# Kernel tuning notes

Measured on AMD Instinct MI355X. Metric: run time of the kernel, lower is better.

## Reference

```python
import jax, jax.numpy as jnp
import numpy as np

B, N, C, H, TR = 2, 5000, 256, 8, 2
M = N // TR  # reduced KV length from Conv1d(data_len, data_len//tr, 1)
DK = C // H


def setup_inputs() -> dict:
    key = jax.random.key(0)
    ks = jax.random.split(key, 10)
    s = 0.02
    return {
        "x": jax.random.normal(ks[0], (B, N, C), jnp.float32),
        "Wq": jax.random.normal(ks[1], (C, C), jnp.float32) * s,
        "bq": jnp.zeros((C,), jnp.float32),
        "Wk": jax.random.normal(ks[2], (C, C), jnp.float32) * s,
        "bk": jnp.zeros((C,), jnp.float32),
        "Wv": jax.random.normal(ks[3], (C, C), jnp.float32) * s,
        "bv": jnp.zeros((C,), jnp.float32),
        "Wc": jax.random.normal(ks[4], (M, N), jnp.float32) * (1.0 / np.sqrt(N)),
        "bc": jnp.zeros((M,), jnp.float32),
        "gamma": jnp.ones((C,), jnp.float32),
        "beta": jnp.zeros((C,), jnp.float32),
    }


def _layernorm(x, gamma, beta, eps=1e-5):
    mu = jnp.mean(x, axis=-1, keepdims=True)
    var = jnp.mean(jnp.square(x - mu), axis=-1, keepdims=True)
    return gamma * (x - mu) * jax.lax.rsqrt(var + eps) + beta


def reference(x, Wq, bq, Wk, bk, Wv, bv, Wc, bc, gamma, beta):
    b, n, c = x.shape
    # Q projection: (B, H, N, DK)
    q = (x @ Wq.T + bq).reshape(b, n, H, DK).transpose(0, 2, 1, 3)
    # Spatial reduction: Conv1d with kernel size 1 over the N (channel) dim,
    # then LayerNorm over feature dim C
    x_ = jnp.einsum('mn,bnc->bmc', Wc, x) + bc[None, :, None]
    x_ = _layernorm(x_, gamma, beta)
    k = (x_ @ Wk.T + bk).reshape(b, -1, H, DK).transpose(0, 2, 1, 3)  # (B,H,M,DK)
    v = (x_ @ Wv.T + bv).reshape(b, -1, H, DK).transpose(0, 2, 1, 3)  # (B,H,M,DK)
    # Naive attention (full score matrix, as in the original module)
    scores = jnp.einsum('bhnd,bhmd->bhnm', q, k) / jnp.sqrt(jnp.asarray(DK, x.dtype))
    p = jax.nn.softmax(scores, axis=-1)
    out = jnp.einsum('bhnm,bhmd->bhnd', p, v)
    # note: output_linear is declared in __init__ but never applied in forward
    return out.transpose(0, 2, 1, 3).reshape(b, n, c)
```

## Files before the change

kernel.cpp:

```cpp
#include <hip/hip_runtime.h>
#include <hip/hip_bf16.h>
#include <hip/hip_fp16.h>
#include <math.h>

constexpr int B = 2;
constexpr int N = 5000;
constexpr int C = 256;
constexpr int H = 8;
constexpr int DK = 32;
constexpr int M = 2500;
constexpr int MP = 2512;
constexpr int KSTEPS = 157;
constexpr int SPLIT = 8;
constexpr int MTILES = 79;
constexpr float QSCALE = 0.2550598692503365f;

typedef __attribute__((ext_vector_type(8))) short bf16x8;
typedef __attribute__((ext_vector_type(4))) float f32x4;

static __device__ __forceinline__ ushort f2bf(float f) {
  __hip_bfloat16 h = __float2bfloat16(f);
  return *reinterpret_cast<ushort*>(&h);
}

static __device__ __forceinline__ float fastexp2(float x) {
#if __has_builtin(__builtin_amdgcn_exp2f)
  return __builtin_amdgcn_exp2f(x);
#else
  return exp2f(x);
#endif
}

__global__ __launch_bounds__(256) void wcast(const float* __restrict__ Wq,
                                             const float* __restrict__ Wk,
                                             const float* __restrict__ Wv,
                                             ushort* __restrict__ W16) {
  const float* src = (blockIdx.y == 0) ? Wq : (blockIdx.y == 1) ? Wk : Wv;
  const int idx = blockIdx.x * 1024 + threadIdx.x * 4;
  const float4 v = *reinterpret_cast<const float4*>(src + idx);
  ushort4 o;
  o.x = f2bf(v.x); o.y = f2bf(v.y); o.z = f2bf(v.z); o.w = f2bf(v.w);
  *reinterpret_cast<ushort4*>(W16 + (size_t)blockIdx.y * C * C + idx) = o;
}

__global__ __launch_bounds__(256) void xt_cast(const float* __restrict__ x,
                                               ushort* __restrict__ xTt,
                                               ushort* __restrict__ xb16) {
  const int n0 = blockIdx.x * 64, c0 = blockIdx.y * 64, b = blockIdx.z;
  const int tid = threadIdx.x;
  __shared__ ushort T[64][68];
  const float* xb = x + (size_t)b * N * C;
#pragma unroll
  for (int i = 0; i < 4; ++i) {
    const int nl = (tid >> 4) + i * 16;
    const int cg = (tid & 15) * 4;
    float4 v = {0.f, 0.f, 0.f, 0.f};
    const bool ok = (n0 + nl) < N;
    if (ok) v = *reinterpret_cast<const float4*>(xb + (size_t)(n0 + nl) * C + c0 + cg);
    ushort4 u;
    u.x = f2bf(v.x); u.y = f2bf(v.y); u.z = f2bf(v.z); u.w = f2bf(v.w);
    T[nl][cg + 0] = u.x; T[nl][cg + 1] = u.y; T[nl][cg + 2] = u.z; T[nl][cg + 3] = u.w;
    if (ok)
      *reinterpret_cast<ushort4*>(xb16 + ((size_t)b * N + n0 + nl) * C + c0 + cg) = u;
  }
  __syncthreads();
  ushort* ob = xTt + (size_t)b * KSTEPS * C * 32;
  const int cl = tid & 63, ng = tid >> 6;
#pragma unroll
  for (int j = 0; j < 2; ++j) {
    const int nstart = ng * 16 + j * 8;
    const int n = n0 + nstart;
    if (n >= KSTEPS * 32) continue;
    const int ks = n >> 5, kk = n & 31;
    ushort vals[8];
#pragma unroll
    for (int jj = 0; jj < 8; ++jj) vals[jj] = T[nstart + jj][cl];
    *reinterpret_cast<bf16x8*>(ob + ((size_t)ks * C + (c0 + cl)) * 32 + kk) =
        *reinterpret_cast<const bf16x8*>(vals);
  }
}

__global__ __launch_bounds__(256) void conv_mfma(const float* __restrict__ Wc,
                                                 const ushort* __restrict__ xTt,
                                                 ushort* __restrict__ xpart) {
  const int s = blockIdx.x & 7;
  const int mt = blockIdx.x >> 3;
  const int m0 = mt * 32;
  const int tid = threadIdx.x, w = tid >> 6, l = tid & 63;
  const int lr = l & 15, lg = l >> 4;
  f32x4 acc[16];
#pragma unroll
  for (int i = 0; i < 16; ++i) acc[i] = (f32x4){0.f, 0.f, 0.f, 0.f};
  const int row0 = m0 + lr, row1 = m0 + 16 + lr;
  const bool ok0 = row0 < M, ok1 = row1 < M;
  const float* ap0 = Wc + (size_t)(ok0 ? row0 : 0) * N + lg * 8;
  const float* ap1 = Wc + (size_t)(ok1 ? row1 : 0) * N + lg * 8;
  const int crow = w * 64 + lr;

#pragma unroll 2
  for (int ks = s; ks < KSTEPS; ks += SPLIT) {
    const int n0 = ks * 32;
    const bool kok = (n0 + lg * 8) < N;
    bf16x8 a0 = {0, 0, 0, 0, 0, 0, 0, 0}, a1 = {0, 0, 0, 0, 0, 0, 0, 0};
    if (ok0 && kok) {
      const float4 v0 = *reinterpret_cast<const float4*>(ap0 + n0);
      const float4 v1 = *reinterpret_cast<const float4*>(ap0 + n0 + 4);
      ushort u[8];
      u[0] = f2bf(v0.x); u[1] = f2bf(v0.y); u[2] = f2bf(v0.z); u[3] = f2bf(v0.w);
      u[4] = f2bf(v1.x); u[5] = f2bf(v1.y); u[6] = f2bf(v1.z); u[7] = f2bf(v1.w);
      a0 = *reinterpret_cast<const bf16x8*>(u);
    }
    if (ok1 && kok) {
      const float4 v0 = *reinterpret_cast<const float4*>(ap1 + n0);
      const float4 v1 = *reinterpret_cast<const float4*>(ap1 + n0 + 4);
      ushort u[8];
      u[0] = f2bf(v0.x); u[1] = f2bf(v0.y); u[2] = f2bf(v0.z); u[3] = f2bf(v0.w);
      u[4] = f2bf(v1.x); u[5] = f2bf(v1.y); u[6] = f2bf(v1.z); u[7] = f2bf(v1.w);
      a1 = *reinterpret_cast<const bf16x8*>(u);
    }
    bf16x8 bf[8];
#pragma unroll
    for (int ct = 0; ct < 4; ++ct)
#pragma unroll
      for (int bb = 0; bb < 2; ++bb)
        bf[ct * 2 + bb] = *reinterpret_cast<const bf16x8*>(
            xTt + (((size_t)bb * KSTEPS + ks) * C + crow + ct * 16) * 32 + lg * 8);
#pragma unroll
    for (int ct = 0; ct < 4; ++ct)
#pragma unroll
      for (int bb = 0; bb < 2; ++bb) {
        acc[(0 * 4 + ct) * 2 + bb] =
            __builtin_amdgcn_mfma_f32_16x16x32_bf16(a0, bf[ct * 2 + bb], acc[(0 * 4 + ct) * 2 + bb], 0, 0, 0);
        acc[(1 * 4 + ct) * 2 + bb] =
            __builtin_amdgcn_mfma_f32_16x16x32_bf16(a1, bf[ct * 2 + bb], acc[(1 * 4 + ct) * 2 + bb], 0, 0, 0);
      }
  }

#pragma unroll
  for (int mf = 0; mf < 2; ++mf)
#pragma unroll
    for (int ct = 0; ct < 4; ++ct)
#pragma unroll
      for (int bb = 0; bb < 2; ++bb)
#pragma unroll
        for (int i = 0; i < 4; ++i) {
          const int m = m0 + mf * 16 + lg * 4 + i;
          if (m < M) {
            const __half hv = __float2half(acc[(mf * 4 + ct) * 2 + bb][i]);
            xpart[(((size_t)s * B + bb) * M + m) * C + w * 64 + ct * 16 + lr] =
                *reinterpret_cast<const ushort*>(&hv);
          }
        }
}

__global__ __launch_bounds__(256) void ln_kernel(const ushort* __restrict__ xp,
                                                 const float* __restrict__ bc,
                                                 const float* __restrict__ gamma,
                                                 const float* __restrict__ beta,
                                                 ushort* __restrict__ xr16) {
  const int row = blockIdx.x;
  const int tid = threadIdx.x;
  const int b = row / M, m = row - b * M;
  const size_t base = (size_t)row * C;
  float v = bc[m];
#pragma unroll
  for (int s = 0; s < SPLIT; ++s) {
    const ushort us = xp[(((size_t)s * B + b) * M + m) * C + tid];
    v += __half2float(*reinterpret_cast<const __half*>(&us));
  }
  __shared__ float red[8];
  float sum = v;
#pragma unroll
  for (int o = 32; o >= 1; o >>= 1) sum += __shfl_xor(sum, o);
  if ((tid & 63) == 0) red[tid >> 6] = sum;
  __syncthreads();
  const float mu = (red[0] + red[1] + red[2] + red[3]) * (1.f / C);
  const float d = v - mu;
  float s2 = d * d;
#pragma unroll
  for (int o = 32; o >= 1; o >>= 1) s2 += __shfl_xor(s2, o);
  if ((tid & 63) == 0) red[4 + (tid >> 6)] = s2;
  __syncthreads();
  const float var = (red[4] + red[5] + red[6] + red[7]) * (1.f / C);
  xr16[base + tid] = f2bf(gamma[tid] * d * rsqrtf(var + 1e-5f) + beta[tid]);
}

__global__ __launch_bounds__(256) void proj_all(const ushort* __restrict__ xb16,
                                                const ushort* __restrict__ xr16,
                                                const ushort* __restrict__ W16,
                                                const float* __restrict__ bq,
                                                const float* __restrict__ bk,
                                                const float* __restrict__ bv,
                                                ushort* __restrict__ qb,
                                                ushort* __restrict__ kb,
                                                ushort* __restrict__ vt) {
  const int z = blockIdx.z;
  const int R = (z == 0) ? N : M;
  const int totalRows = B * R;
  if (blockIdx.x * 64 >= totalRows) return;
  const ushort* xin = (z == 0) ? xb16 : xr16;
  const ushort* W = W16 + (size_t)z * C * C;
  const float* bias = (z == 0) ? bq : (z == 1) ? bk : bv;
  const int tid = threadIdx.x, w = tid >> 6, l = tid & 63;
  const int lr = l & 15, lg = l >> 4;
  const int r0 = blockIdx.x * 64 + w * 16;
  const int c0 = blockIdx.y * 64;
  const int arow = r0 + lr;
  const bool aok = arow < totalRows;
  f32x4 acc[4] = {{0.f,0.f,0.f,0.f},{0.f,0.f,0.f,0.f},{0.f,0.f,0.f,0.f},{0.f,0.f,0.f,0.f}};
#pragma unroll
  for (int ks = 0; ks < 8; ++ks) {
    bf16x8 af = {0, 0, 0, 0, 0, 0, 0, 0};
    if (aok) af = *reinterpret_cast<const bf16x8*>(xin + (size_t)arow * C + ks * 32 + lg * 8);
#pragma unroll
    for (int ct = 0; ct < 4; ++ct) {
      const bf16x8 bf =
          *reinterpret_cast<const bf16x8*>(W + (size_t)(c0 + ct * 16 + lr) * C + ks * 32 + lg * 8);
      acc[ct] = __builtin_amdgcn_mfma_f32_16x16x32_bf16(af, bf, acc[ct], 0, 0, 0);
    }
  }
#pragma unroll
  for (int ct = 0; ct < 4; ++ct) {
    const int c = c0 + ct * 16 + lr;
    const int h = c >> 5, d = c & 31;
    const float bi = bias[c];
#pragma unroll
    for (int i = 0; i < 4; ++i) {
      const int row = r0 + lg * 4 + i;
      if (row >= totalRows) continue;
      const int bb = (row >= R) ? 1 : 0;
      const int rr = row - bb * R;
      float val = acc[ct][i] + bi;
      if (z == 0) {
        val *= QSCALE;
        qb[(((size_t)bb * H + h) * N + rr) * DK + d] = f2bf(val);
      } else if (z == 1) {
        kb[(((size_t)bb * H + h) * M + rr) * DK + d] = f2bf(val);
      } else {
        vt[(((size_t)bb * H + h) * DK + d) * MP + rr] = f2bf(val);
      }
    }
  }
}

__global__ __launch_bounds__(256) void attn9(const ushort* __restrict__ q,
                                             const ushort* __restrict__ kk,
                                             const ushort* __restrict__ vt,
                                             float* __restrict__ o0,
                                             float* __restrict__ o1,
                                             float* __restrict__ ps0,
                                             float* __restrict__ ps1) {
  const int qt = blockIdx.x, h = blockIdx.y, z = blockIdx.z;
  const int b = z >> 1, half = z & 1;
  const int tid = threadIdx.x, w = tid >> 6, l = tid & 63;
  const int lr = l & 15, lg = l >> 4;
  const int n0 = qt * 128 + w * 32;
  __shared__ ushort Plds[4][2][16][72];
  const ushort* qp = q + (size_t)(b * H + h) * N * DK;
  const ushort* kp = kk + (size_t)(b * H + h) * M * DK;
  const ushort* vp = vt + (size_t)(b * H + h) * DK * MP;
  float* op = half ? o1 : o0;
  float* ps = half ? ps1 : ps0;

  bf16x8 qf0 = {0, 0, 0, 0, 0, 0, 0, 0}, qf1 = {0, 0, 0, 0, 0, 0, 0, 0};
  if (n0 + lr < N) qf0 = *reinterpret_cast<const bf16x8*>(qp + (size_t)(n0 + lr) * DK + lg * 8);
  if (n0 + 16 + lr < N)
    qf1 = *reinterpret_cast<const bf16x8*>(qp + (size_t)(n0 + 16 + lr) * DK + lg * 8);

  f32x4 O0[2] = {{0.f, 0.f, 0.f, 0.f}, {0.f, 0.f, 0.f, 0.f}};
  f32x4 O1[2] = {{0.f, 0.f, 0.f, 0.f}, {0.f, 0.f, 0.f, 0.f}};
  float ps0r = 0.f, ps1r = 0.f;

  const int tbeg = half ? 20 : 0;
  const int tend = half ? 40 : 20;
#pragma unroll 1
  for (int t = tbeg; t < tend; ++t) {
    const int m0 = t * 64;
    const bool full = (m0 + 64) <= M;
    bf16x8 kf[4];
#pragma unroll
    for (int ct = 0; ct < 4; ++ct) {
      const int mr = m0 + ct * 16 + lr;
      if (full || mr < M)
        kf[ct] = *reinterpret_cast<const bf16x8*>(kp + (size_t)mr * DK + lg * 8);
      else
        kf[ct] = (bf16x8){0, 0, 0, 0, 0, 0, 0, 0};
    }
    bf16x8 vf[4];
#pragma unroll
    for (int dt = 0; dt < 2; ++dt) {
      const ushort* vb = vp + (size_t)(dt * 16 + lr) * MP + m0 + lg * 8;
      vf[dt * 2 + 0] = *reinterpret_cast<const bf16x8*>(vb);
      vf[dt * 2 + 1] = *reinterpret_cast<const bf16x8*>(vb + 32);
    }
#pragma unroll
    for (int ct = 0; ct < 4; ++ct) {
      const f32x4 s0 =
          __builtin_amdgcn_mfma_f32_16x16x32_bf16(kf[ct], qf0, (f32x4){0.f, 0.f, 0.f, 0.f}, 0, 0, 0);
      const f32x4 s1 =
          __builtin_amdgcn_mfma_f32_16x16x32_bf16(kf[ct], qf1, (f32x4){0.f, 0.f, 0.f, 0.f}, 0, 0, 0);
      float p0[4], p1[4];
#pragma unroll
      for (int i = 0; i < 4; ++i) {
        const bool mok = full || (m0 + ct * 16 + lg * 4 + i) < M;
        p0[i] = mok ? fastexp2(s0[i]) : 0.f;
        p1[i] = mok ? fastexp2(s1[i]) : 0.f;
        ps0r += p0[i];
        ps1r += p1[i];
      }
      __hip_bfloat162 a01 = __float22bfloat162_rn(make_float2(p0[0], p0[1]));
      __hip_bfloat162 a23 = __float22bfloat162_rn(make_float2(p0[2], p0[3]));
      uint2 u0;
      u0.x = *reinterpret_cast<unsigned*>(&a01);
      u0.y = *reinterpret_cast<unsigned*>(&a23);
      *reinterpret_cast<uint2*>(&Plds[w][0][lr][ct * 16 + lg * 4]) = u0;
      __hip_bfloat162 b01 = __float22bfloat162_rn(make_float2(p1[0], p1[1]));
      __hip_bfloat162 b23 = __float22bfloat162_rn(make_float2(p1[2], p1[3]));
      uint2 u1;
      u1.x = *reinterpret_cast<unsigned*>(&b01);
      u1.y = *reinterpret_cast<unsigned*>(&b23);
      *reinterpret_cast<uint2*>(&Plds[w][1][lr][ct * 16 + lg * 4]) = u1;
    }
    const bf16x8 pa00 = *reinterpret_cast<const bf16x8*>(&Plds[w][0][lr][lg * 8]);
    const bf16x8 pa01 = *reinterpret_cast<const bf16x8*>(&Plds[w][0][lr][32 + lg * 8]);
    const bf16x8 pa10 = *reinterpret_cast<const bf16x8*>(&Plds[w][1][lr][lg * 8]);
    const bf16x8 pa11 = *reinterpret_cast<const bf16x8*>(&Plds[w][1][lr][32 + lg * 8]);
#pragma unroll
    for (int dt = 0; dt < 2; ++dt) {
      O0[dt] = __builtin_amdgcn_mfma_f32_16x16x32_bf16(pa00, vf[dt * 2 + 0], O0[dt], 0, 0, 0);
      O0[dt] = __builtin_amdgcn_mfma_f32_16x16x32_bf16(pa01, vf[dt * 2 + 1], O0[dt], 0, 0, 0);
      O1[dt] = __builtin_amdgcn_mfma_f32_16x16x32_bf16(pa10, vf[dt * 2 + 0], O1[dt], 0, 0, 0);
      O1[dt] = __builtin_amdgcn_mfma_f32_16x16x32_bf16(pa11, vf[dt * 2 + 1], O1[dt], 0, 0, 0);
    }
  }

  ps0r += __shfl_xor(ps0r, 16);
  ps0r += __shfl_xor(ps0r, 32);
  ps1r += __shfl_xor(ps1r, 16);
  ps1r += __shfl_xor(ps1r, 32);
  if (lg == 0) {
    const size_t pbase = ((size_t)b * H + h) * N;
    if (n0 + lr < N) ps[pbase + n0 + lr] = ps0r;
    if (n0 + 16 + lr < N) ps[pbase + n0 + 16 + lr] = ps1r;
  }
#pragma unroll
  for (int i = 0; i < 4; ++i) {
    const int r0q = n0 + lg * 4 + i;
    const int r1q = n0 + 16 + lg * 4 + i;
    if (r0q < N) {
      float* ob = op + ((size_t)b * N + r0q) * C + h * DK + lr;
      ob[0] = O0[0][i];
      ob[16] = O0[1][i];
    }
    if (r1q < N) {
      float* ob = op + ((size_t)b * N + r1q) * C + h * DK + lr;
      ob[0] = O1[0][i];
      ob[16] = O1[1][i];
    }
  }
}

__global__ __launch_bounds__(256) void attn_combine(float* __restrict__ out,
                                                    const float* __restrict__ o1,
                                                    const float* __restrict__ ps0,
                                                    const float* __restrict__ ps1) {
  const int row = blockIdx.x;
  const int c = threadIdx.x;
  const int b = row / N, n = row - b * N;
  const size_t pidx = ((size_t)b * H + (c >> 5)) * N + n;
  const float denom = ps0[pidx] + ps1[pidx];
  const size_t idx = (size_t)row * C + c;
  out[idx] = (out[idx] + o1[idx]) / denom;
}

extern "C" void kernel_launch(void* const* d_in, const int* in_sizes, int n_in,
                              void* d_out, int out_size, void* d_ws, size_t ws_size,
                              hipStream_t stream) {
  (void)in_sizes; (void)n_in; (void)out_size; (void)ws_size;
  const float* x     = (const float*)d_in[0];
  const float* Wq    = (const float*)d_in[1];
  const float* bq    = (const float*)d_in[2];
  const float* Wk    = (const float*)d_in[3];
  const float* bk    = (const float*)d_in[4];
  const float* Wv    = (const float*)d_in[5];
  const float* bv    = (const float*)d_in[6];
  const float* Wc    = (const float*)d_in[7];
  const float* bc    = (const float*)d_in[8];
  const float* gamma = (const float*)d_in[9];
  const float* beta  = (const float*)d_in[10];
  float* out = (float*)d_out;

  char* wsb = (char*)d_ws;
  ushort* xpart = (ushort*)wsb;
  ushort* qb = (ushort*)wsb;
  ushort* kb = (ushort*)(wsb + 5120000);
  ushort* vt = (ushort*)(wsb + 7680000);
  float* ps0 = (float*)(wsb + 10400000);
  float* ps1 = (float*)(wsb + 10720000);
  char* p = wsb + 20480000;
  ushort* xTt  = (ushort*)p;
  ushort* xr16 = (ushort*)p;
  float* o1 = (float*)p;
  p += 5144576;
  ushort* xb16 = (ushort*)p; p += 5120000;
  ushort* W16  = (ushort*)p;

  wcast<<<dim3(64, 3), 256, 0, stream>>>(Wq, Wk, Wv, W16);
  xt_cast<<<dim3((N + 63) / 64, C / 64, B), 256, 0, stream>>>(x, xTt, xb16);
  conv_mfma<<<dim3(MTILES * SPLIT), 256, 0, stream>>>(Wc, xTt, xpart);
  ln_kernel<<<dim3(B * M), 256, 0, stream>>>(xpart, bc, gamma, beta, xr16);
  (void)hipMemsetAsync(vt, 0, (size_t)B * H * DK * MP * 2 + 4096, stream);
  proj_all<<<dim3((B * N + 63) / 64, C / 64, 3), 256, 0, stream>>>(xb16, xr16, W16, bq, bk, bv,
                                                                   qb, kb, vt);
  attn9<<<dim3((N + 127) / 128, H, B * 2), 256, 0, stream>>>(qb, kb, vt, out, o1, ps0, ps1);
  attn_combine<<<dim3(B * N), 256, 0, stream>>>(out, o1, ps0, ps1);
}
```

Measured before the change: 177.6 us.

## Compute softmax row sums via MFMA with ones row; peel tail tile; widen conv blocks

The attention kernel appends a row of ones to the transposed V buffer, so the P·V MFMA also produces the softmax denominators. This replaces the per-element scalar sums and cross-lane shuffles. The main loop now handles only full 64-wide KV tiles without bounds masks, and the partial last tile is peeled out into a separate block. The conv kernel uses 512-thread blocks, each wave covering 32 channels instead of 64, which halves its accumulator registers. The cost is extra MFMAs, a larger V buffer, one extra small kernel to write the ones row, and a bigger memset.

```diff
diff --git a/kernel.cpp b/kernel.cpp
--- a/kernel.cpp
+++ b/kernel.cpp
@@ -10,6 +10,7 @@
 constexpr int DK = 32;
 constexpr int M = 2500;
 constexpr int MP = 2512;
+constexpr int VROWS = 48;
 constexpr int KSTEPS = 157;
 constexpr int SPLIT = 8;
 constexpr int MTILES = 79;
@@ -41,6 +42,12 @@
   ushort4 o;
   o.x = f2bf(v.x); o.y = f2bf(v.y); o.z = f2bf(v.z); o.w = f2bf(v.w);
   *reinterpret_cast<ushort4*>(W16 + (size_t)blockIdx.y * C * C + idx) = o;
+}
+
+__global__ __launch_bounds__(256) void vt_ones(ushort* __restrict__ vt) {
+  const int bh = blockIdx.y;
+  const int j = blockIdx.x * 256 + threadIdx.x;
+  if (j < MP) vt[((size_t)bh * VROWS + 32) * MP + j] = 0x3F80;
 }
 
 __global__ __launch_bounds__(256) void xt_cast(const float* __restrict__ x,
@@ -80,7 +87,7 @@
   }
 }
 
-__global__ __launch_bounds__(256) void conv_mfma(const float* __restrict__ Wc,
+__global__ __launch_bounds__(512) void conv_mfma(const float* __restrict__ Wc,
                                                  const ushort* __restrict__ xTt,
                                                  ushort* __restrict__ xpart) {
   const int s = blockIdx.x & 7;
@@ -88,14 +95,14 @@
   const int m0 = mt * 32;
   const int tid = threadIdx.x, w = tid >> 6, l = tid & 63;
   const int lr = l & 15, lg = l >> 4;
-  f32x4 acc[16];
-#pragma unroll
-  for (int i = 0; i < 16; ++i) acc[i] = (f32x4){0.f, 0.f, 0.f, 0.f};
+  f32x4 acc[8];
+#pragma unroll
+  for (int i = 0; i < 8; ++i) acc[i] = (f32x4){0.f, 0.f, 0.f, 0.f};
   const int row0 = m0 + lr, row1 = m0 + 16 + lr;
   const bool ok0 = row0 < M, ok1 = row1 < M;
   const float* ap0 = Wc + (size_t)(ok0 ? row0 : 0) * N + lg * 8;
   const float* ap1 = Wc + (size_t)(ok1 ? row1 : 0) * N + lg * 8;
-  const int crow = w * 64 + lr;
+  const int crow = w * 32 + lr;
 
 #pragma unroll 2
   for (int ks = s; ks < KSTEPS; ks += SPLIT) {
@@ -118,36 +125,36 @@
       u[4] = f2bf(v1.x); u[5] = f2bf(v1.y); u[6] = f2bf(v1.z); u[7] = f2bf(v1.w);
       a1 = *reinterpret_cast<const bf16x8*>(u);
     }
-    bf16x8 bf[8];
-#pragma unroll
-    for (int ct = 0; ct < 4; ++ct)
+    bf16x8 bf[4];
+#pragma unroll
+    for (int ct = 0; ct < 2; ++ct)
 #pragma unroll
       for (int bb = 0; bb < 2; ++bb)
         bf[ct * 2 + bb] = *reinterpret_cast<const bf16x8*>(
             xTt + (((size_t)bb * KSTEPS + ks) * C + crow + ct * 16) * 32 + lg * 8);
 #pragma unroll
-    for (int ct = 0; ct < 4; ++ct)
+    for (int ct = 0; ct < 2; ++ct)
 #pragma unroll
       for (int bb = 0; bb < 2; ++bb) {
-        acc[(0 * 4 + ct) * 2 + bb] =
-            __builtin_amdgcn_mfma_f32_16x16x32_bf16(a0, bf[ct * 2 + bb], acc[(0 * 4 + ct) * 2 + bb], 0, 0, 0);
-        acc[(1 * 4 + ct) * 2 + bb] =
-            __builtin_amdgcn_mfma_f32_16x16x32_bf16(a1, bf[ct * 2 + bb], acc[(1 * 4 + ct) * 2 + bb], 0, 0, 0);
+        acc[(0 * 2 + ct) * 2 + bb] =
+            __builtin_amdgcn_mfma_f32_16x16x32_bf16(a0, bf[ct * 2 + bb], acc[(0 * 2 + ct) * 2 + bb], 0, 0, 0);
+        acc[(1 * 2 + ct) * 2 + bb] =
+            __builtin_amdgcn_mfma_f32_16x16x32_bf16(a1, bf[ct * 2 + bb], acc[(1 * 2 + ct) * 2 + bb], 0, 0, 0);
       }
   }
 
 #pragma unroll
   for (int mf = 0; mf < 2; ++mf)
 #pragma unroll
-    for (int ct = 0; ct < 4; ++ct)
+    for (int ct = 0; ct < 2; ++ct)
 #pragma unroll
       for (int bb = 0; bb < 2; ++bb)
 #pragma unroll
         for (int i = 0; i < 4; ++i) {
           const int m = m0 + mf * 16 + lg * 4 + i;
           if (m < M) {
-            const __half hv = __float2half(acc[(mf * 4 + ct) * 2 + bb][i]);
-            xpart[(((size_t)s * B + bb) * M + m) * C + w * 64 + ct * 16 + lr] =
+            const __half hv = __float2half(acc[(mf * 2 + ct) * 2 + bb][i]);
+            xpart[(((size_t)s * B + bb) * M + m) * C + w * 32 + ct * 16 + lr] =
                 *reinterpret_cast<const ushort*>(&hv);
           }
         }
@@ -237,19 +244,19 @@
       } else if (z == 1) {
         kb[(((size_t)bb * H + h) * M + rr) * DK + d] = f2bf(val);
       } else {
-        vt[(((size_t)bb * H + h) * DK + d) * MP + rr] = f2bf(val);
+        vt[(((size_t)bb * H + h) * VROWS + d) * MP + rr] = f2bf(val);
       }
     }
   }
 }
 
-__global__ __launch_bounds__(256) void attn9(const ushort* __restrict__ q,
-                                             const ushort* __restrict__ kk,
-                                             const ushort* __restrict__ vt,
-                                             float* __restrict__ o0,
-                                             float* __restrict__ o1,
-                                             float* __restrict__ ps0,
-                                             float* __restrict__ ps1) {
+__global__ __launch_bounds__(256) void attn10(const ushort* __restrict__ q,
+                                              const ushort* __restrict__ kk,
+                                              const ushort* __restrict__ vt,
+                                              float* __restrict__ o0,
+                                              float* __restrict__ o1,
+                                              float* __restrict__ ps0,
+                                              float* __restrict__ ps1) {
   const int qt = blockIdx.x, h = blockIdx.y, z = blockIdx.z;
   const int b = z >> 1, half = z & 1;
   const int tid = threadIdx.x, w = tid >> 6, l = tid & 63;
@@ -258,7 +265,7 @@
   __shared__ ushort Plds[4][2][16][72];
   const ushort* qp = q + (size_t)(b * H + h) * N * DK;
   const ushort* kp = kk + (size_t)(b * H + h) * M * DK;
-  const ushort* vp = vt + (size_t)(b * H + h) * DK * MP;
+  const ushort* vp = vt + (size_t)(b * H + h) * VROWS * MP;
   float* op = half ? o1 : o0;
   float* ps = half ? ps1 : ps0;
 
@@ -269,29 +276,85 @@
 
   f32x4 O0[2] = {{0.f, 0.f, 0.f, 0.f}, {0.f, 0.f, 0.f, 0.f}};
   f32x4 O1[2] = {{0.f, 0.f, 0.f, 0.f}, {0.f, 0.f, 0.f, 0.f}};
-  float ps0r = 0.f, ps1r = 0.f;
+  f32x4 O2a = {0.f, 0.f, 0.f, 0.f}, O2b = {0.f, 0.f, 0.f, 0.f};
 
   const int tbeg = half ? 20 : 0;
-  const int tend = half ? 40 : 20;
+  const int tendf = half ? 39 : 20;
 #pragma unroll 1
-  for (int t = tbeg; t < tend; ++t) {
+  for (int t = tbeg; t < tendf; ++t) {
     const int m0 = t * 64;
-    const bool full = (m0 + 64) <= M;
     bf16x8 kf[4];
 #pragma unroll
-    for (int ct = 0; ct < 4; ++ct) {
-      const int mr = m0 + ct * 16 + lr;
-      if (full || mr < M)
-        kf[ct] = *reinterpret_cast<const bf16x8*>(kp + (size_t)mr * DK + lg * 8);
-      else
-        kf[ct] = (bf16x8){0, 0, 0, 0, 0, 0, 0, 0};
-    }
-    bf16x8 vf[4];
+    for (int ct = 0; ct < 4; ++ct)
+      kf[ct] = *reinterpret_cast<const bf16x8*>(kp + (size_t)(m0 + ct * 16 + lr) * DK + lg * 8);
+    bf16x8 vf[4], vf2[2];
 #pragma unroll
     for (int dt = 0; dt < 2; ++dt) {
       const ushort* vb = vp + (size_t)(dt * 16 + lr) * MP + m0 + lg * 8;
       vf[dt * 2 + 0] = *reinterpret_cast<const bf16x8*>(vb);
       vf[dt * 2 + 1] = *reinterpret_cast<const bf16x8*>(vb + 32);
+    }
+    {
+      const ushort* vb2 = vp + (size_t)(32 + lr) * MP + m0 + lg * 8;
+      vf2[0] = *reinterpret_cast<const bf16x8*>(vb2);
+      vf2[1] = *reinterpret_cast<const bf16x8*>(vb2 + 32);
+    }
+#pragma unroll
+    for (int ct = 0; ct < 4; ++ct) {
+      const f32x4 s0 =
+          __builtin_amdgcn_mfma_f32_16x16x32_bf16(kf[ct], qf0, (f32x4){0.f, 0.f, 0.f, 0.f}, 0, 0, 0);
+      const f32x4 s1 =
+          __builtin_amdgcn_mfma_f32_16x16x32_bf16(kf[ct], qf1, (f32x4){0.f, 0.f, 0.f, 0.f}, 0, 0, 0);
+      __hip_bfloat162 a01 = __float22bfloat162_rn(make_float2(fastexp2(s0[0]), fastexp2(s0[1])));
+      __hip_bfloat162 a23 = __float22bfloat162_rn(make_float2(fastexp2(s0[2]), fastexp2(s0[3])));
+      uint2 u0;
+      u0.x = *reinterpret_cast<unsigned*>(&a01);
+      u0.y = *reinterpret_cast<unsigned*>(&a23);
+      *reinterpret_cast<uint2*>(&Plds[w][0][lr][ct * 16 + lg * 4]) = u0;
+      __hip_bfloat162 b01 = __float22bfloat162_rn(make_float2(fastexp2(s1[0]), fastexp2(s1[1])));
+      __hip_bfloat162 b23 = __float22bfloat162_rn(make_float2(fastexp2(s1[2]), fastexp2(s1[3])));
+      uint2 u1;
+      u1.x = *reinterpret_cast<unsigned*>(&b01);
+      u1.y = *reinterpret_cast<unsigned*>(&b23);
+      *reinterpret_cast<uint2*>(&Plds[w][1][lr][ct * 16 + lg * 4]) = u1;
+    }
+    const bf16x8 pa00 = *reinterpret_cast<const bf16x8*>(&Plds[w][0][lr][lg * 8]);
+    const bf16x8 pa01 = *reinterpret_cast<const bf16x8*>(&Plds[w][0][lr][32 + lg * 8]);
+    const bf16x8 pa10 = *reinterpret_cast<const bf16x8*>(&Plds[w][1][lr][lg * 8]);
+    const bf16x8 pa11 = *reinterpret_cast<const bf16x8*>(&Plds[w][1][lr][32 + lg * 8]);
+#pragma unroll
+    for (int dt = 0; dt < 2; ++dt) {
+      O0[dt] = __builtin_amdgcn_mfma_f32_16x16x32_bf16(pa00, vf[dt * 2 + 0], O0[dt], 0, 0, 0);
+      O0[dt] = __builtin_amdgcn_mfma_f32_16x16x32_bf16(pa01, vf[dt * 2 + 1], O0[dt], 0, 0, 0);
+      O1[dt] = __builtin_amdgcn_mfma_f32_16x16x32_bf16(pa10, vf[dt * 2 + 0], O1[dt], 0, 0, 0);
+      O1[dt] = __builtin_amdgcn_mfma_f32_16x16x32_bf16(pa11, vf[dt * 2 + 1], O1[dt], 0, 0, 0);
+    }
+    O2a = __builtin_amdgcn_mfma_f32_16x16x32_bf16(pa00, vf2[0], O2a, 0, 0, 0);
+    O2a = __builtin_amdgcn_mfma_f32_16x16x32_bf16(pa01, vf2[1], O2a, 0, 0, 0);
+    O2b = __builtin_amdgcn_mfma_f32_16x16x32_bf16(pa10, vf2[0], O2b, 0, 0, 0);
+    O2b = __builtin_amdgcn_mfma_f32_16x16x32_bf16(pa11, vf2[1], O2b, 0, 0, 0);
+  }
+
+  if (half) {
+    const int m0 = 39 * 64;
+    bf16x8 kf[4];
+#pragma unroll
+    for (int ct = 0; ct < 4; ++ct) {
+      const int mr = m0 + ct * 16 + lr;
+      kf[ct] = (bf16x8){0, 0, 0, 0, 0, 0, 0, 0};
+      if (mr < M) kf[ct] = *reinterpret_cast<const bf16x8*>(kp + (size_t)mr * DK + lg * 8);
+    }
+    bf16x8 vf[4], vf2[2];
+#pragma unroll
+    for (int dt = 0; dt < 2; ++dt) {
+      const ushort* vb = vp + (size_t)(dt * 16 + lr) * MP + m0 + lg * 8;
+      vf[dt * 2 + 0] = *reinterpret_cast<const bf16x8*>(vb);
+      vf[dt * 2 + 1] = *reinterpret_cast<const bf16x8*>(vb + 32);
+    }
+    {
+      const ushort* vb2 = vp + (size_t)(32 + lr) * MP + m0 + lg * 8;
+      vf2[0] = *reinterpret_cast<const bf16x8*>(vb2);
+      vf2[1] = *reinterpret_cast<const bf16x8*>(vb2 + 32);
     }
 #pragma unroll
     for (int ct = 0; ct < 4; ++ct) {
@@ -302,11 +365,9 @@
       float p0[4], p1[4];
 #pragma unroll
       for (int i = 0; i < 4; ++i) {
-        const bool mok = full || (m0 + ct * 16 + lg * 4 + i) < M;
+        const bool mok = (m0 + ct * 16 + lg * 4 + i) < M;
         p0[i] = mok ? fastexp2(s0[i]) : 0.f;
         p1[i] = mok ? fastexp2(s1[i]) : 0.f;
-        ps0r += p0[i];
-        ps1r += p1[i];
       }
       __hip_bfloat162 a01 = __float22bfloat162_rn(make_float2(p0[0], p0[1]));
       __hip_bfloat162 a23 = __float22bfloat162_rn(make_float2(p0[2], p0[3]));
@@ -332,16 +393,21 @@
       O1[dt] = __builtin_amdgcn_mfma_f32_16x16x32_bf16(pa10, vf[dt * 2 + 0], O1[dt], 0, 0, 0);
       O1[dt] = __builtin_amdgcn_mfma_f32_16x16x32_bf16(pa11, vf[dt * 2 + 1], O1[dt], 0, 0, 0);
     }
-  }
-
-  ps0r += __shfl_xor(ps0r, 16);
-  ps0r += __shfl_xor(ps0r, 32);
-  ps1r += __shfl_xor(ps1r, 16);
-  ps1r += __shfl_xor(ps1r, 32);
-  if (lg == 0) {
+    O2a = __builtin_amdgcn_mfma_f32_16x16x32_bf16(pa00, vf2[0], O2a, 0, 0, 0);
+    O2a = __builtin_amdgcn_mfma_f32_16x16x32_bf16(pa01, vf2[1], O2a, 0, 0, 0);
+    O2b = __builtin_amdgcn_mfma_f32_16x16x32_bf16(pa10, vf2[0], O2b, 0, 0, 0);
+    O2b = __builtin_amdgcn_mfma_f32_16x16x32_bf16(pa11, vf2[1], O2b, 0, 0, 0);
+  }
+
+  if (lr == 0) {
     const size_t pbase = ((size_t)b * H + h) * N;
-    if (n0 + lr < N) ps[pbase + n0 + lr] = ps0r;
-    if (n0 + 16 + lr < N) ps[pbase + n0 + 16 + lr] = ps1r;
+#pragma unroll
+    for (int i = 0; i < 4; ++i) {
+      const int q0r = n0 + lg * 4 + i;
+      const int q1r = n0 + 16 + lg * 4 + i;
+      if (q0r < N) ps[pbase + q0r] = O2a[i];
+      if (q1r < N) ps[pbase + q1r] = O2b[i];
+    }
   }
 #pragma unroll
   for (int i = 0; i < 4; ++i) {
@@ -395,8 +461,8 @@
   ushort* qb = (ushort*)wsb;
   ushort* kb = (ushort*)(wsb + 5120000);
   ushort* vt = (ushort*)(wsb + 7680000);
-  float* ps0 = (float*)(wsb + 10400000);
-  float* ps1 = (float*)(wsb + 10720000);
+  float* ps0 = (float*)(wsb + 11600000);
+  float* ps1 = (float*)(wsb + 11920000);
   char* p = wsb + 20480000;
   ushort* xTt  = (ushort*)p;
   ushort* xr16 = (ushort*)p;
@@ -407,11 +473,12 @@
 
   wcast<<<dim3(64, 3), 256, 0, stream>>>(Wq, Wk, Wv, W16);
   xt_cast<<<dim3((N + 63) / 64, C / 64, B), 256, 0, stream>>>(x, xTt, xb16);
-  conv_mfma<<<dim3(MTILES * SPLIT), 256, 0, stream>>>(Wc, xTt, xpart);
+  conv_mfma<<<dim3(MTILES * SPLIT), 512, 0, stream>>>(Wc, xTt, xpart);
   ln_kernel<<<dim3(B * M), 256, 0, stream>>>(xpart, bc, gamma, beta, xr16);
-  (void)hipMemsetAsync(vt, 0, (size_t)B * H * DK * MP * 2 + 4096, stream);
+  (void)hipMemsetAsync(vt, 0, (size_t)B * H * VROWS * MP * 2 + 4096, stream);
+  vt_ones<<<dim3((MP + 255) / 256, B * H), 256, 0, stream>>>(vt);
   proj_all<<<dim3((B * N + 63) / 64, C / 64, 3), 256, 0, stream>>>(xb16, xr16, W16, bq, bk, bv,
                                                                    qb, kb, vt);
-  attn9<<<dim3((N + 127) / 128, H, B * 2), 256, 0, stream>>>(qb, kb, vt, out, o1, ps0, ps1);
+  attn10<<<dim3((N + 127) / 128, H, B * 2), 256, 0, stream>>>(qb, kb, vt, out, o1, ps0, ps1);
   attn_combine<<<dim3(B * N), 256, 0, stream>>>(out, o1, ps0, ps1);
 }
```

After: 191.8 us. +8.0%, slower.
